# Kernel optimization log

Measured on AMD Instinct MI355X. Metric: run time of the kernel, lower is better.

Reference implementation:

```python
import jax, jax.numpy as jnp
import numpy as np

LATENT_SIZE = 1024
WORD_SIZE = 64
NB_WORD = 8192
COMMIT_VQ = 2.5
BATCH = 2048


def setup_inputs() -> dict:
    key = jax.random.key(0)
    k1, k2, k3 = jax.random.split(key, 3)
    z_mean = jax.random.normal(k1, (BATCH, LATENT_SIZE), dtype=jnp.float32)
    z_log_var = jax.random.normal(k2, (BATCH, LATENT_SIZE), dtype=jnp.float32)
    # Embedding initialized uniform(-1/nb_word, 1/nb_word) in the torch module;
    # use normal here for a numerically non-degenerate correctness baseline.
    emb_weight = jax.random.normal(k3, (NB_WORD, WORD_SIZE), dtype=jnp.float32)
    return {"z_mean": z_mean, "z_log_var": z_log_var, "emb_weight": emb_weight}


def reference(z_mean, z_log_var, emb_weight):
    sg = jax.lax.stop_gradient
    input_shape = z_mean.shape
    # (B * latent/word, word)
    z = z_mean.reshape(-1, LATENT_SIZE // WORD_SIZE, WORD_SIZE)
    z_flat = z.reshape(-1, WORD_SIZE)
    # squared euclidean distances: (N, nb_word)
    distances = (
        jnp.sum(z_flat ** 2, axis=1, keepdims=True)
        + jnp.sum(emb_weight ** 2, axis=1)
        - 2.0 * jnp.einsum("bd,nd->bn", z_flat, emb_weight)
    )
    min_idx = jnp.argmin(distances, axis=1)  # (N,)
    z_q = emb_weight[min_idx].reshape(z.shape)  # gather codebook vectors
    loss = (
        jnp.mean((sg(z_q) - z) ** 2)
        + COMMIT_VQ * jnp.mean((z_q - sg(z)) ** 2)
    )
    z_q_st = z + sg(z_q - z)  # straight-through estimator
    return z_q_st.reshape(input_shape), loss
```

## Files before the change

### kernel.cpp

```cpp
#include <hip/hip_runtime.h>
#include <math.h>

#define LATENT   1024
#define WORD     64
#define NB_WORD  8192
#define BATCH    2048
#define NROWS    (BATCH * LATENT / WORD)
#define NELEM    (BATCH * LATENT)

#define NCHUNK   8
#define CWCHUNK  (NB_WORD / NCHUNK)
#define TPC      (CWCHUNK / 16)
#define NTILE    (NB_WORD / 16)
#define PKTS     (NTILE * 6 * 64)

typedef __attribute__((ext_vector_type(8))) __bf16 bf16x8;
typedef __attribute__((ext_vector_type(4))) float  f32x4;

__global__ __launch_bounds__(256) void vq_prep_kernel(
    const float* __restrict__ emb, float* __restrict__ e2,
    bf16x8* __restrict__ epack) {
    int m = blockIdx.x * 256 + threadIdx.x;
    int tile = m >> 4, l15 = m & 15;
    float s0 = 0.f, s1 = 0.f, s2 = 0.f, s3 = 0.f;
#pragma unroll
    for (int Ks = 0; Ks < 2; ++Ks) {
#pragma unroll
        for (int q = 0; q < 4; ++q) {
            const float4* s4 = reinterpret_cast<const float4*>(
                emb + (size_t)m * WORD + Ks * 32 + q * 8);
            float4 a = s4[0], b = s4[1];
            float tv[8] = {a.x, a.y, a.z, a.w, b.x, b.y, b.z, b.w};
            bf16x8 oh, om, ol;
#pragma unroll
            for (int e = 0; e < 8; ++e) {
                float v = tv[e];
                if ((e & 3) == 0) s0 = fmaf(v, v, s0);
                else if ((e & 3) == 1) s1 = fmaf(v, v, s1);
                else if ((e & 3) == 2) s2 = fmaf(v, v, s2);
                else s3 = fmaf(v, v, s3);
                __bf16 h  = (__bf16)v;
                float r1  = v - (float)h;
                __bf16 mm = (__bf16)r1;
                float r2  = r1 - (float)mm;
                __bf16 lo = (__bf16)r2;
                oh[e] = h; om[e] = mm; ol[e] = lo;
            }
            size_t base = ((size_t)tile * 6) * 64 + q * 16 + l15;
            epack[base + (size_t)(0 * 2 + Ks) * 64] = oh;
            epack[base + (size_t)(1 * 2 + Ks) * 64] = om;
            epack[base + (size_t)(2 * 2 + Ks) * 64] = ol;
        }
    }
    e2[m] = (s0 + s1) + (s2 + s3);
}

__device__ __forceinline__ void gload_lds16(const char* g, char* l) {
    __builtin_amdgcn_global_load_lds(
        (const __attribute__((address_space(1))) void*)g,
        (__attribute__((address_space(3))) void*)l, 16, 0, 0);
}

#define MFMA16 __builtin_amdgcn_mfma_f32_16x16x32_bf16
#define SBAR() __builtin_amdgcn_sched_barrier(0)

__global__ __launch_bounds__(256)
__attribute__((amdgpu_waves_per_eu(3, 3)))
void vq_argmin_kernel(
    const float* __restrict__ z, const bf16x8* __restrict__ epack,
    const float* __restrict__ e2, unsigned long long* __restrict__ best) {

    {
        int ph = blockIdx.x & 3;
        if (ph == 1) __builtin_amdgcn_s_sleep(2);
        else if (ph == 2) __builtin_amdgcn_s_sleep(4);
        else if (ph == 3) __builtin_amdgcn_s_sleep(6);
    }

    __shared__ __align__(16) char le[2 * 6144];

    const int tid   = threadIdx.x;
    const int lane  = tid & 63;
    const int wband = tid >> 6;
    const int l15   = lane & 15;
    const int l4    = lane >> 4;
    const int rowbase   = blockIdx.x * 128 + wband * 32;
    const int tile0     = blockIdx.y * TPC;
    const int chunkbase = blockIdx.y * CWCHUNK;
    const float* e2g    = e2 + chunkbase;
    const int off       = (blockIdx.x & 15) * 4;

    bf16x8 A[2][2][3];
    const float4* zf4 = reinterpret_cast<const float4*>(z);
#pragma unroll
    for (int mt = 0; mt < 2; ++mt) {
        int row = rowbase + mt * 16 + l15;
#pragma unroll
        for (int Ks = 0; Ks < 2; ++Ks) {
            float4 v0 = zf4[(size_t)row * 16 + Ks * 8 + l4 * 2];
            float4 v1 = zf4[(size_t)row * 16 + Ks * 8 + l4 * 2 + 1];
            float tv[8] = {v0.x, v0.y, v0.z, v0.w, v1.x, v1.y, v1.z, v1.w};
#pragma unroll
            for (int e = 0; e < 8; ++e) {
                float v = tv[e];
                __bf16 h  = (__bf16)v;
                float r1  = v - (float)h;
                __bf16 m  = (__bf16)r1;
                float r2  = r1 - (float)m;
                __bf16 lo = (__bf16)r2;
                A[mt][Ks][0][e] = h;
                A[mt][Ks][1][e] = m;
                A[mt][Ks][2][e] = lo;
            }
        }
    }

    {
        const char* src = (const char*)epack + (size_t)(tile0 + off) * 6144;
        gload_lds16(src + wband * 1024 + lane * 16, le + wband * 1024);
        if (wband < 2)
            gload_lds16(src + (4 + wband) * 1024 + lane * 16,
                        le + (4 + wband) * 1024);
    }

    float bestd[8] = {INFINITY, INFINITY, INFINITY, INFINITY,
                      INFINITY, INFINITY, INFINITY, INFINITY};
    int   bt[8]    = {0, 0, 0, 0, 0, 0, 0, 0};

    f32x4 x00, x01, x10, x11;
    f32x4 y00 = {0.f,0.f,0.f,0.f}, y01 = {0.f,0.f,0.f,0.f};
    f32x4 y10 = {0.f,0.f,0.f,0.f}, y11 = {0.f,0.f,0.f,0.f};
    float e2x, e2y = INFINITY;

#define FOLD1(P00,P01,P10,P11, E2P, TP, V)                                  \
    do {                                                                    \
        float d0_ = fmaf(-2.0f, P00[V] + P01[V], E2P);                      \
        if (d0_ < bestd[V])     { bestd[V]     = d0_; bt[V]     = (TP); }   \
        float d1_ = fmaf(-2.0f, P10[V] + P11[V], E2P);                      \
        if (d1_ < bestd[4+(V)]) { bestd[4+(V)] = d1_; bt[4+(V)] = (TP); }   \
    } while (0)

#define GROUP(SPL, B0, B1, C00,C01,C10,C11)                                 \
    C00 = MFMA16(A[0][0][SPL], B0, C00, 0, 0, 0);                           \
    C10 = MFMA16(A[1][0][SPL], B0, C10, 0, 0, 0);                           \
    C01 = MFMA16(A[0][1][SPL], B1, C01, 0, 0, 0);                           \
    C11 = MFMA16(A[1][1][SPL], B1, C11, 0, 0, 0);

#define PHASE(BUFOFF, C00,C01,C10,C11, P00,P01,P10,P11, E2C, E2P, TCUR, TNXT, TP) \
    {                                                                       \
        asm volatile("s_waitcnt vmcnt(0)" ::: "memory");                    \
        SBAR();                                                             \
        __builtin_amdgcn_s_barrier();          \
        const char* bb = le + (BUFOFF) + lane * 16;                         \
        bf16x8 Bh0 = *reinterpret_cast<const bf16x8*>(bb);                  \
        bf16x8 Bh1 = *reinterpret_cast<const bf16x8*>(bb + 1024);           \
        bf16x8 Bm0 = *reinterpret_cast<const bf16x8*>(bb + 2048);           \
        bf16x8 Bm1 = *reinterpret_cast<const bf16x8*>(bb + 3072);           \
        bf16x8 Bl0 = *reinterpret_cast<const bf16x8*>(bb + 4096);           \
        bf16x8 Bl1 = *reinterpret_cast<const bf16x8*>(bb + 5120);           \
        const char* srcn = (const char*)epack +                             \
                           (size_t)(tile0 + (TNXT)) * 6144;                 \
        char* dstn = le + ((BUFOFF) ^ 6144);                                \
        gload_lds16(srcn + wband * 1024 + lane * 16, dstn + wband * 1024);  \
        if (wband < 2)                                                      \
            gload_lds16(srcn + (4 + wband) * 1024 + lane * 16,              \
                        dstn + (4 + wband) * 1024);                         \
        E2C = e2g[(TCUR) * 16 + l15];                                       \
        __builtin_amdgcn_s_setprio(1);                                      \
        SBAR();                                                             \
                \
        FOLD1(P00,P01,P10,P11, E2P, TP, 0);                                 \
        FOLD1(P00,P01,P10,P11, E2P, TP, 1);                                 \
        C00 = (f32x4){0.f,0.f,0.f,0.f};                                     \
        C01 = (f32x4){0.f,0.f,0.f,0.f};                                     \
        C10 = (f32x4){0.f,0.f,0.f,0.f};                                     \
        C11 = (f32x4){0.f,0.f,0.f,0.f};                                     \
        SBAR();                                                             \
        GROUP(0, Bh0, Bh1, C00,C01,C10,C11)                         \
        SBAR();                                                             \
        FOLD1(P00,P01,P10,P11, E2P, TP, 2);                                 \
        SBAR();                                                             \
        GROUP(1, Bh0, Bh1, C00,C01,C10,C11)                         \
        SBAR();                                                             \
        FOLD1(P00,P01,P10,P11, E2P, TP, 3);                                 \
        SBAR();                                                             \
        GROUP(2, Bh0, Bh1, C00,C01,C10,C11)                         \
        GROUP(1, Bm0, Bm1, C00,C01,C10,C11)                         \
        GROUP(0, Bm0, Bm1, C00,C01,C10,C11)                         \
        GROUP(0, Bl0, Bl1, C00,C01,C10,C11)                         \
        __builtin_amdgcn_s_setprio(0);                                      \
    }

    int t0 = off;
    int tp = 0;
    for (int tt = 0; tt < TPC; tt += 2) {
        int t1 = t0 + 1; if (t1 >= TPC) t1 -= TPC;
        int t2 = t1 + 1; if (t2 >= TPC) t2 -= TPC;
        PHASE(0,    x00,x01,x10,x11, y00,y01,y10,y11, e2x, e2y, t0, t1, tp);
        PHASE(6144, y00,y01,y10,y11, x00,x01,x10,x11, e2y, e2x, t1, t2, t0);
        tp = t1;
        t0 = t2;
    }
#undef PHASE

    asm volatile("s_waitcnt vmcnt(0)" ::: "memory");
    FOLD1(y00,y01,y10,y11, e2y, tp, 0);
    FOLD1(y00,y01,y10,y11, e2y, tp, 1);
    FOLD1(y00,y01,y10,y11, e2y, tp, 2);
    FOLD1(y00,y01,y10,y11, e2y, tp, 3);
#undef FOLD1
#undef GROUP

#pragma unroll
    for (int mt = 0; mt < 2; ++mt) {
#pragma unroll
        for (int v = 0; v < 4; ++v) {
            float bd = bestd[mt * 4 + v];
            int   cw = chunkbase + bt[mt * 4 + v] * 16 + l15;
            unsigned db = __float_as_uint(bd);
            db = (db & 0x80000000u) ? ~db : (db | 0x80000000u);
            unsigned long long key =
                ((unsigned long long)db << 32) | (unsigned)cw;
#pragma unroll
            for (int off2 = 1; off2 < 16; off2 <<= 1) {
                unsigned long long o = __shfl_xor(key, off2);
                key = (o < key) ? o : key;
            }
            if (l15 == 0)
                atomicMin(&best[rowbase + mt * 16 + l4 * 4 + v], key);
        }
    }
}

__global__ __launch_bounds__(256) void vq_out_kernel(
    const float* __restrict__ z, const float* __restrict__ emb,
    const unsigned long long* __restrict__ best,
    float* __restrict__ out, float* __restrict__ lsum) {
    const int base = (blockIdx.x * 256 + threadIdx.x) * 8;
    const int row  = base >> 6;
    const int m    = (int)(best[row] & 0xFFFFFFFFull);

    const float4* zp = reinterpret_cast<const float4*>(z + base);
    const float4* qp = reinterpret_cast<const float4*>(emb + (size_t)m * WORD + (base & 63));
    float4* op = reinterpret_cast<float4*>(out + base);

    float s = 0.f;
#pragma unroll
    for (int i = 0; i < 2; ++i) {
        float4 zv = zp[i];
        float4 qv = qp[i];
        float dx = qv.x - zv.x, dy = qv.y - zv.y, dz = qv.z - zv.z, dw = qv.w - zv.w;
        float4 ov;
        ov.x = zv.x + dx; ov.y = zv.y + dy; ov.z = zv.z + dz; ov.w = zv.w + dw;
        op[i] = ov;
        s += dx*dx + dy*dy + dz*dz + dw*dw;
    }

#pragma unroll
    for (int off = 32; off > 0; off >>= 1) s += __shfl_down(s, off);
    __shared__ float wsum[4];
    int lane = threadIdx.x & 63, wid = threadIdx.x >> 6;
    if (lane == 0) wsum[wid] = s;
    __syncthreads();
    if (threadIdx.x == 0)
        atomicAdd(lsum, (wsum[0] + wsum[1]) + (wsum[2] + wsum[3]));
}

__global__ void vq_loss_kernel(const float* __restrict__ lsum,
                               float* __restrict__ loss_out) {
    float mean = lsum[0] * (1.0f / (float)NELEM);
    loss_out[0] = mean + 2.5f * mean;
}

extern "C" void kernel_launch(void* const* d_in, const int* in_sizes, int n_in,
                              void* d_out, int out_size, void* d_ws, size_t ws_size,
                              hipStream_t stream) {
    const float* z   = (const float*)d_in[0];
    const float* emb = (const float*)d_in[2];
    float* out = (float*)d_out;

    bf16x8* epack = (bf16x8*)d_ws;
    float*  e2    = (float*)((char*)d_ws + (size_t)PKTS * 16);
    unsigned long long* best =
        (unsigned long long*)((char*)e2 + NB_WORD * sizeof(float));
    float* lsum = (float*)((char*)best + NROWS * sizeof(unsigned long long));

    hipMemsetAsync(best, 0xFF, NROWS * sizeof(unsigned long long), stream);
    hipMemsetAsync(lsum, 0, sizeof(float), stream);

    vq_prep_kernel<<<NB_WORD / 256, 256, 0, stream>>>(emb, e2, epack);
    vq_argmin_kernel<<<dim3(NROWS / 128, NCHUNK), 256, 0, stream>>>(
        z, epack, e2, best);
    vq_out_kernel<<<NELEM / (256 * 8), 256, 0, stream>>>(z, emb, best, out, lsum);
    vq_loss_kernel<<<1, 1, 0, stream>>>(lsum, out + NELEM);
}
```

Baseline: 200.1 us.

## Process two codebook tiles per phase with serial accumulators and raise occupancy

Each pipeline phase now loads and computes two 16-codeword tiles from a 12 KB double buffer instead of one, halving the number of barriers per codebook chunk. The separate K-half accumulators are merged into one accumulator chain per row-tile, and the deferred fold of the previous tile's distances is replaced by an immediate fold after the MFMAs. Occupancy is raised from 3 to 4 waves per EU so other waves can hide the now-serial MFMA dependency chains and the fold latency. The trade-offs are a larger LDS footprint, dependent back-to-back MFMAs on the same accumulator, and tighter register limits at the higher occupancy.

```diff
diff --git a/kernel.cpp b/kernel.cpp
--- a/kernel.cpp
+++ b/kernel.cpp
@@ -62,10 +62,9 @@
 }
 
 #define MFMA16 __builtin_amdgcn_mfma_f32_16x16x32_bf16
-#define SBAR() __builtin_amdgcn_sched_barrier(0)
 
 __global__ __launch_bounds__(256)
-__attribute__((amdgpu_waves_per_eu(3, 3)))
+__attribute__((amdgpu_waves_per_eu(4, 4)))
 void vq_argmin_kernel(
     const float* __restrict__ z, const bf16x8* __restrict__ epack,
     const float* __restrict__ e2, unsigned long long* __restrict__ best) {
@@ -77,7 +76,7 @@
         else if (ph == 3) __builtin_amdgcn_s_sleep(6);
     }
 
-    __shared__ __align__(16) char le[2 * 6144];
+    __shared__ __align__(16) char le[2 * 12288];
 
     const int tid   = threadIdx.x;
     const int lane  = tid & 63;
@@ -117,99 +116,102 @@
 
     {
         const char* src = (const char*)epack + (size_t)(tile0 + off) * 6144;
-        gload_lds16(src + wband * 1024 + lane * 16, le + wband * 1024);
-        if (wband < 2)
-            gload_lds16(src + (4 + wband) * 1024 + lane * 16,
-                        le + (4 + wband) * 1024);
-    }
+        gload_lds16(src + wband * 1024 + lane * 16,       le + wband * 1024);
+        gload_lds16(src + (4 + wband) * 1024 + lane * 16, le + (4 + wband) * 1024);
+        gload_lds16(src + (8 + wband) * 1024 + lane * 16, le + (8 + wband) * 1024);
+    }
+    float e2nA = e2g[off * 16 + l15];
+    float e2nB = e2g[(off + 1) * 16 + l15];
 
     float bestd[8] = {INFINITY, INFINITY, INFINITY, INFINITY,
                       INFINITY, INFINITY, INFINITY, INFINITY};
     int   bt[8]    = {0, 0, 0, 0, 0, 0, 0, 0};
 
-    f32x4 x00, x01, x10, x11;
-    f32x4 y00 = {0.f,0.f,0.f,0.f}, y01 = {0.f,0.f,0.f,0.f};
-    f32x4 y10 = {0.f,0.f,0.f,0.f}, y11 = {0.f,0.f,0.f,0.f};
-    float e2x, e2y = INFINITY;
-
-#define FOLD1(P00,P01,P10,P11, E2P, TP, V)                                  \
-    do {                                                                    \
-        float d0_ = fmaf(-2.0f, P00[V] + P01[V], E2P);                      \
-        if (d0_ < bestd[V])     { bestd[V]     = d0_; bt[V]     = (TP); }   \
-        float d1_ = fmaf(-2.0f, P10[V] + P11[V], E2P);                      \
-        if (d1_ < bestd[4+(V)]) { bestd[4+(V)] = d1_; bt[4+(V)] = (TP); }   \
-    } while (0)
-
-#define GROUP(SPL, B0, B1, C00,C01,C10,C11)                                 \
-    C00 = MFMA16(A[0][0][SPL], B0, C00, 0, 0, 0);                           \
-    C10 = MFMA16(A[1][0][SPL], B0, C10, 0, 0, 0);                           \
-    C01 = MFMA16(A[0][1][SPL], B1, C01, 0, 0, 0);                           \
-    C11 = MFMA16(A[1][1][SPL], B1, C11, 0, 0, 0);
-
-#define PHASE(BUFOFF, C00,C01,C10,C11, P00,P01,P10,P11, E2C, E2P, TCUR, TNXT, TP) \
+#define CLUSTER(AC0, AC1, Bh0, Bh1, Bm0, Bm1, Bl0, Bl1)                     \
+    AC0 = MFMA16(A[0][0][0], Bh0, AC0, 0, 0, 0);                            \
+    AC1 = MFMA16(A[1][0][0], Bh0, AC1, 0, 0, 0);                            \
+    AC0 = MFMA16(A[0][0][1], Bh0, AC0, 0, 0, 0);                            \
+    AC1 = MFMA16(A[1][0][1], Bh0, AC1, 0, 0, 0);                            \
+    AC0 = MFMA16(A[0][0][2], Bh0, AC0, 0, 0, 0);                            \
+    AC1 = MFMA16(A[1][0][2], Bh0, AC1, 0, 0, 0);                            \
+    AC0 = MFMA16(A[0][0][0], Bm0, AC0, 0, 0, 0);                            \
+    AC1 = MFMA16(A[1][0][0], Bm0, AC1, 0, 0, 0);                            \
+    AC0 = MFMA16(A[0][0][1], Bm0, AC0, 0, 0, 0);                            \
+    AC1 = MFMA16(A[1][0][1], Bm0, AC1, 0, 0, 0);                            \
+    AC0 = MFMA16(A[0][0][0], Bl0, AC0, 0, 0, 0);                            \
+    AC1 = MFMA16(A[1][0][0], Bl0, AC1, 0, 0, 0);                            \
+    AC0 = MFMA16(A[0][1][0], Bh1, AC0, 0, 0, 0);                            \
+    AC1 = MFMA16(A[1][1][0], Bh1, AC1, 0, 0, 0);                            \
+    AC0 = MFMA16(A[0][1][1], Bh1, AC0, 0, 0, 0);                            \
+    AC1 = MFMA16(A[1][1][1], Bh1, AC1, 0, 0, 0);                            \
+    AC0 = MFMA16(A[0][1][2], Bh1, AC0, 0, 0, 0);                            \
+    AC1 = MFMA16(A[1][1][2], Bh1, AC1, 0, 0, 0);                            \
+    AC0 = MFMA16(A[0][1][0], Bm1, AC0, 0, 0, 0);                            \
+    AC1 = MFMA16(A[1][1][0], Bm1, AC1, 0, 0, 0);                            \
+    AC0 = MFMA16(A[0][1][1], Bm1, AC0, 0, 0, 0);                            \
+    AC1 = MFMA16(A[1][1][1], Bm1, AC1, 0, 0, 0);                            \
+    AC0 = MFMA16(A[0][1][0], Bl1, AC0, 0, 0, 0);                            \
+    AC1 = MFMA16(A[1][1][0], Bl1, AC1, 0, 0, 0);
+
+#define FOLD(AC0, AC1, E2V, T)                                              \
+    _Pragma("unroll")                                                       \
+    for (int v = 0; v < 4; ++v) {                                           \
+        float d0 = fmaf(-2.0f, AC0[v], E2V);                                \
+        if (d0 < bestd[v])     { bestd[v]     = d0; bt[v]     = (T); }      \
+        float d1 = fmaf(-2.0f, AC1[v], E2V);                                \
+        if (d1 < bestd[4 + v]) { bestd[4 + v] = d1; bt[4 + v] = (T); }      \
+    }
+
+#define PHASE(BUFOFF, TA, TB, TNA, TNB)                                     \
     {                                                                       \
         asm volatile("s_waitcnt vmcnt(0)" ::: "memory");                    \
-        SBAR();                                                             \
+        __builtin_amdgcn_sched_barrier(0);                                  \
         __builtin_amdgcn_s_barrier();          \
+        const float e2cA = e2nA, e2cB = e2nB;                               \
+        const char* srcn = (const char*)epack +                             \
+                           (size_t)(tile0 + (TNA)) * 6144;                  \
+        char* dstn = le + ((BUFOFF) ^ 12288);                               \
+        gload_lds16(srcn + wband * 1024 + lane * 16, dstn + wband * 1024);  \
+        gload_lds16(srcn + (4 + wband) * 1024 + lane * 16,                  \
+                    dstn + (4 + wband) * 1024);                             \
+        gload_lds16(srcn + (8 + wband) * 1024 + lane * 16,                  \
+                    dstn + (8 + wband) * 1024);                             \
+        e2nA = e2g[(TNA) * 16 + l15];                                       \
+        e2nB = e2g[(TNB) * 16 + l15];                                       \
         const char* bb = le + (BUFOFF) + lane * 16;                         \
-        bf16x8 Bh0 = *reinterpret_cast<const bf16x8*>(bb);                  \
-        bf16x8 Bh1 = *reinterpret_cast<const bf16x8*>(bb + 1024);           \
-        bf16x8 Bm0 = *reinterpret_cast<const bf16x8*>(bb + 2048);           \
-        bf16x8 Bm1 = *reinterpret_cast<const bf16x8*>(bb + 3072);           \
-        bf16x8 Bl0 = *reinterpret_cast<const bf16x8*>(bb + 4096);           \
-        bf16x8 Bl1 = *reinterpret_cast<const bf16x8*>(bb + 5120);           \
-        const char* srcn = (const char*)epack +                             \
-                           (size_t)(tile0 + (TNXT)) * 6144;                 \
-        char* dstn = le + ((BUFOFF) ^ 6144);                                \
-        gload_lds16(srcn + wband * 1024 + lane * 16, dstn + wband * 1024);  \
-        if (wband < 2)                                                      \
-            gload_lds16(srcn + (4 + wband) * 1024 + lane * 16,              \
-                        dstn + (4 + wband) * 1024);                         \
-        E2C = e2g[(TCUR) * 16 + l15];                                       \
+        bf16x8 Ah0 = *reinterpret_cast<const bf16x8*>(bb);                  \
+        bf16x8 Ah1 = *reinterpret_cast<const bf16x8*>(bb + 1024);           \
+        bf16x8 Am0 = *reinterpret_cast<const bf16x8*>(bb + 2048);           \
+        bf16x8 Am1 = *reinterpret_cast<const bf16x8*>(bb + 3072);           \
+        bf16x8 Al0 = *reinterpret_cast<const bf16x8*>(bb + 4096);           \
+        bf16x8 Al1 = *reinterpret_cast<const bf16x8*>(bb + 5120);           \
+        bf16x8 Bh0 = *reinterpret_cast<const bf16x8*>(bb + 6144);           \
+        bf16x8 Bh1 = *reinterpret_cast<const bf16x8*>(bb + 7168);           \
+        bf16x8 Bm0 = *reinterpret_cast<const bf16x8*>(bb + 8192);           \
+        bf16x8 Bm1 = *reinterpret_cast<const bf16x8*>(bb + 9216);           \
+        bf16x8 Bl0 = *reinterpret_cast<const bf16x8*>(bb + 10240);          \
+        bf16x8 Bl1 = *reinterpret_cast<const bf16x8*>(bb + 11264);          \
+        f32x4 a0 = {0.f,0.f,0.f,0.f}, a1 = {0.f,0.f,0.f,0.f};               \
+        f32x4 b0 = {0.f,0.f,0.f,0.f}, b1 = {0.f,0.f,0.f,0.f};               \
         __builtin_amdgcn_s_setprio(1);                                      \
-        SBAR();                                                             \
-                \
-        FOLD1(P00,P01,P10,P11, E2P, TP, 0);                                 \
-        FOLD1(P00,P01,P10,P11, E2P, TP, 1);                                 \
-        C00 = (f32x4){0.f,0.f,0.f,0.f};                                     \
-        C01 = (f32x4){0.f,0.f,0.f,0.f};                                     \
-        C10 = (f32x4){0.f,0.f,0.f,0.f};                                     \
-        C11 = (f32x4){0.f,0.f,0.f,0.f};                                     \
-        SBAR();                                                             \
-        GROUP(0, Bh0, Bh1, C00,C01,C10,C11)                         \
-        SBAR();                                                             \
-        FOLD1(P00,P01,P10,P11, E2P, TP, 2);                                 \
-        SBAR();                                                             \
-        GROUP(1, Bh0, Bh1, C00,C01,C10,C11)                         \
-        SBAR();                                                             \
-        FOLD1(P00,P01,P10,P11, E2P, TP, 3);                                 \
-        SBAR();                                                             \
-        GROUP(2, Bh0, Bh1, C00,C01,C10,C11)                         \
-        GROUP(1, Bm0, Bm1, C00,C01,C10,C11)                         \
-        GROUP(0, Bm0, Bm1, C00,C01,C10,C11)                         \
-        GROUP(0, Bl0, Bl1, C00,C01,C10,C11)                         \
+        CLUSTER(a0, a1, Ah0, Ah1, Am0, Am1, Al0, Al1)                       \
+        CLUSTER(b0, b1, Bh0, Bh1, Bm0, Bm1, Bl0, Bl1)                       \
         __builtin_amdgcn_s_setprio(0);                                      \
+        FOLD(a0, a1, e2cA, TA)              \
+        FOLD(b0, b1, e2cB, TB)                                              \
     }
 
     int t0 = off;
-    int tp = 0;
-    for (int tt = 0; tt < TPC; tt += 2) {
-        int t1 = t0 + 1; if (t1 >= TPC) t1 -= TPC;
-        int t2 = t1 + 1; if (t2 >= TPC) t2 -= TPC;
-        PHASE(0,    x00,x01,x10,x11, y00,y01,y10,y11, e2x, e2y, t0, t1, tp);
-        PHASE(6144, y00,y01,y10,y11, x00,x01,x10,x11, e2y, e2x, t1, t2, t0);
-        tp = t1;
-        t0 = t2;
+    for (int tt = 0; tt < TPC; tt += 4) {
+        const int p2 = (t0 + 2) & (TPC - 1);
+        const int p4 = (t0 + 4) & (TPC - 1);
+        PHASE(0,     t0, t0 + 1, p2, p2 + 1);
+        PHASE(12288, p2, p2 + 1, p4, p4 + 1);
+        t0 = p4;
     }
 #undef PHASE
-
-    asm volatile("s_waitcnt vmcnt(0)" ::: "memory");
-    FOLD1(y00,y01,y10,y11, e2y, tp, 0);
-    FOLD1(y00,y01,y10,y11, e2y, tp, 1);
-    FOLD1(y00,y01,y10,y11, e2y, tp, 2);
-    FOLD1(y00,y01,y10,y11, e2y, tp, 3);
-#undef FOLD1
-#undef GROUP
+#undef CLUSTER
+#undef FOLD
 
 #pragma unroll
     for (int mt = 0; mt < 2; ++mt) {
```

Result: slower. 370.6 us (+85.2%).
